# Kernel tuning notes

Hardware: AMD Instinct MI355X
Metric: run time of the kernel (lower is better)

Reference implementation:

```python
import jax, jax.numpy as jnp
import numpy as np

# ---------- constants ----------
EPS = 1e-5
_rng = np.random.default_rng(0)
_P = _rng.normal(size=(8, 3))
_P /= np.linalg.norm(_P, axis=1, keepdims=True)

def _y2_np(p):
    x, y, z = p[:, 0], p[:, 1], p[:, 2]
    return np.stack([x * y, y * z, 3 * z * z - 1, x * z, x * x - y * y], axis=-1)

_A2 = np.linalg.pinv(_y2_np(_P)).astype(np.float32)  # [5,8]
P_C = jnp.asarray(_P.astype(np.float32))
A2_C = jnp.asarray(_A2)
NORM_CONST = np.float32(1.0 / np.sqrt(20.0))  # avg_num_neighbors ** -0.5
# res update (buffer zeros, not learnable): sigmoid(0)=0.5
_U = 0.5
C_OLD = np.float32(1.0 / np.sqrt(_U * _U + 1.0))
C_NEW = np.float32(_U * C_OLD)


def _y2(p):  # real l=2 monomial basis on unit vectors
    x, y, z = p[..., 0], p[..., 1], p[..., 2]
    return jnp.stack([x * y, y * z, 3.0 * z * z - 1.0, x * z, x * x - y * y], axis=-1)


def _frame(v):  # [E,3] -> R [E,3,3] with R @ v_hat = z
    n = v / jnp.linalg.norm(v, axis=-1, keepdims=True)
    z = jnp.array([0.0, 0.0, 1.0], v.dtype)
    xa = jnp.array([1.0, 0.0, 0.0], v.dtype)
    a = jnp.where(jnp.abs(n[:, 2:3]) < 0.99, z, xa)
    e1 = jnp.cross(a, n)
    e1 = e1 / jnp.linalg.norm(e1, axis=-1, keepdims=True)
    e2 = jnp.cross(n, e1)
    return jnp.stack([e1, e2, n], axis=1)


def _wigner_d2(R):  # [E,3,3] -> D2 [E,5,5] via sample-point fit
    pts = jnp.einsum('pj,eij->epi', P_C, R)  # R @ p_k, [E,8,3]
    M = _y2(pts)  # [E,8,5] = Y_P @ D^T
    Dt = jnp.einsum('ap,epb->eab', A2_C, M)  # [E,5,5]
    return jnp.swapaxes(Dt, 1, 2)


def _sln(x, w0, b0, w1, w2):  # separable equivariant layernorm, 32x0e+16x1e+8x2e
    s = x[:, :32]
    v1 = x[:, 32:80].reshape(-1, 16, 3)
    v2 = x[:, 80:120].reshape(-1, 8, 5)
    mu = jnp.mean(s, axis=-1, keepdims=True)
    var = jnp.mean((s - mu) ** 2, axis=-1, keepdims=True)
    s = (s - mu) * jax.lax.rsqrt(var + EPS) * w0 + b0
    var1 = jnp.mean(v1 ** 2, axis=(1, 2))  # degree-balanced component variance
    var2 = jnp.mean(v2 ** 2, axis=(1, 2))
    inv = jax.lax.rsqrt(0.5 * (var1 + var2) + EPS)[:, None, None]
    v1 = v1 * inv * w1[None, :, None]
    v2 = v2 * inv * w2[None, :, None]
    return jnp.concatenate([s, v1.reshape(-1, 48), v2.reshape(-1, 40)], axis=-1)


def _ir_linear(x, W0, b0, W1, W2):  # irreps-wise linear 32x0e+16x1e+8x2e -> same
    s = x[:, :32] @ (W0 / np.sqrt(32.0)) + b0
    v1 = jnp.einsum('eui,uv->evi', x[:, 32:80].reshape(-1, 16, 3), W1) / np.sqrt(16.0)
    v2 = jnp.einsum('eui,uv->evi', x[:, 80:120].reshape(-1, 8, 5), W2) / np.sqrt(8.0)
    return jnp.concatenate([s, v1.reshape(-1, 48), v2.reshape(-1, 40)], axis=-1)


def _so2(x_cat, R, D2f, D2b, w):  # SO2 linear with per-edge dynamic weights
    E = x_cat.shape[0]
    w0 = w[:, :8960].reshape(E, 112, 80)
    w1r = w[:, 8960:10112].reshape(E, 48, 24)
    w1i = w[:, 10112:11264].reshape(E, 48, 24)
    w2r = w[:, 11264:11392].reshape(E, 16, 8)
    w2i = w[:, 11392:11520].reshape(E, 16, 8)
    # split concatenated [in + hidden] blocks
    s = jnp.concatenate([x_cat[:, :32], x_cat[:, 120:152]], axis=-1)  # [E,64]
    v1 = jnp.concatenate([x_cat[:, 32:80].reshape(E, 16, 3),
                          x_cat[:, 152:200].reshape(E, 16, 3)], axis=1)  # [E,32,3]
    v2 = jnp.concatenate([x_cat[:, 80:120].reshape(E, 8, 5),
                          x_cat[:, 200:240].reshape(E, 16 // 2, 5)], axis=1)  # [E,16,5]
    # rotate into edge-aligned frame
    v1 = jnp.einsum('eij,euj->eui', R, v1)
    v2 = jnp.einsum('eij,euj->eui', D2f, v2)
    in0 = jnp.concatenate([s, v1[:, :, 1], v2[:, :, 2]], axis=-1)   # m=0, [E,112]
    inn1 = jnp.concatenate([v1[:, :, 0], v2[:, :, 1]], axis=-1)     # m=-1, [E,48]
    inp1 = jnp.concatenate([v1[:, :, 2], v2[:, :, 3]], axis=-1)     # m=+1
    inn2 = v2[:, :, 0]  # m=-2
    inp2 = v2[:, :, 4]  # m=+2
    out0 = jnp.einsum('ei,eio->eo', in0, w0) / np.sqrt(112.0)
    op1 = (jnp.einsum('ei,eio->eo', inp1, w1r) - jnp.einsum('ei,eio->eo', inn1, w1i)) / np.sqrt(48.0)
    on1 = (jnp.einsum('ei,eio->eo', inn1, w1r) + jnp.einsum('ei,eio->eo', inp1, w1i)) / np.sqrt(48.0)
    op2 = (jnp.einsum('ei,eio->eo', inp2, w2r) - jnp.einsum('ei,eio->eo', inn2, w2i)) / np.sqrt(16.0)
    on2 = (jnp.einsum('ei,eio->eo', inn2, w2r) + jnp.einsum('ei,eio->eo', inp2, w2i)) / np.sqrt(16.0)
    s_out = out0[:, :56]
    y1 = jnp.stack([on1[:, :16], out0[:, 56:72], op1[:, :16]], axis=-1)  # [E,16,3]
    y2o = jnp.stack([on2, on1[:, 16:24], out0[:, 72:80], op1[:, 16:24], op2], axis=-1)  # [E,8,5]
    # rotate back
    y1 = jnp.einsum('eij,euj->eui', jnp.swapaxes(R, 1, 2), y1)
    y2o = jnp.einsum('eij,euj->eui', D2b, y2o)
    return jnp.concatenate([s_out, y1.reshape(E, 48), y2o.reshape(E, 40)], axis=-1)  # [E,144]


def _gate(m):  # 32x0e scalars | 24x0e gates | 16x1e+8x2e gated
    s = jax.nn.silu(m[:, :32])
    g = jax.nn.sigmoid(m[:, 32:56])
    v1 = m[:, 56:104].reshape(-1, 16, 3) * g[:, :16, None]
    v2 = m[:, 104:144].reshape(-1, 8, 5) * g[:, 16:24, None]
    return jnp.concatenate([s, v1.reshape(-1, 48), v2.reshape(-1, 40)], axis=-1)


def _env(m, we):  # E3ElementLinear: per-mul elementwise weights
    s = m[:, :32] * we[:, :32]
    v1 = m[:, 32:80].reshape(-1, 16, 3) * we[:, 32:48, None]
    v2 = m[:, 80:120].reshape(-1, 8, 5) * we[:, 48:56, None]
    return jnp.concatenate([s, v1.reshape(-1, 48), v2.reshape(-1, 40)], axis=-1)


def setup_inputs() -> dict:
    key = jax.random.key(0)
    ks = jax.random.split(key, 16)
    N, E, L = 512, 10240, 128
    inp = {
        'latents': jax.random.normal(ks[0], (E, L), jnp.float32),
        'node_features': jax.random.normal(ks[1], (N, 120), jnp.float32),
        'hidden_features': jax.random.normal(ks[2], (E, 120), jnp.float32),
        'node_onehot': jnp.ones((N, 16), jnp.float32),
        'edge_vector': jax.random.normal(ks[3], (E, 3), jnp.float32),
        'W_tp': jax.random.normal(ks[4], (L, 11520), jnp.float32),
        'W_env': jax.random.normal(ks[5], (L, 56), jnp.float32),
        'sln_w0': jnp.ones((32,), jnp.float32),
        'sln_b0': jnp.zeros((32,), jnp.float32),
        'sln_w1': jnp.ones((16,), jnp.float32),
        'sln_w2': jnp.ones((8,), jnp.float32),
        'Wp0': jax.random.normal(ks[6], (32, 32), jnp.float32),
        'bp0': jnp.zeros((32,), jnp.float32),
        'Wp1': jax.random.normal(ks[7], (16, 16), jnp.float32),
        'Wp2': jax.random.normal(ks[8], (8, 8), jnp.float32),
        'Wr0': jax.random.normal(ks[9], (32, 32), jnp.float32),
        'br0': jnp.zeros((32,), jnp.float32),
        'Wr1': jax.random.normal(ks[10], (16, 16), jnp.float32),
        'Wr2': jax.random.normal(ks[11], (8, 8), jnp.float32),
        'atom_type': jax.random.randint(ks[12], (N,), 0, 10, jnp.int32),
        'edge_index': jax.random.randint(ks[13], (2, E), 0, N, jnp.int32),
        'active_edges': jnp.arange(E, dtype=jnp.int32),
    }
    return inp


def reference(latents, node_features, hidden_features, node_onehot, edge_vector,
              W_tp, W_env, sln_w0, sln_b0, sln_w1, sln_w2,
              Wp0, bp0, Wp1, Wp2, Wr0, br0, Wr1, Wr2,
              atom_type, edge_index, active_edges):
    n_nodes = node_features.shape[0]
    center = edge_index[0][active_edges]
    nf = _sln(node_features, sln_w0, sln_b0, sln_w1, sln_w2)
    x_cat = jnp.concatenate([nf[center], hidden_features], axis=-1)  # [E,240]
    v = edge_vector[active_edges]
    R = _frame(v)
    D2f = _wigner_d2(R)
    D2b = _wigner_d2(jnp.swapaxes(R, 1, 2))
    wdyn = latents @ (W_tp / np.sqrt(128.0))  # per-edge dynamic SO2 weights
    msg = _so2(x_cat, R, D2f, D2b, wdyn)
    msg = _gate(msg)
    msg = _ir_linear(msg, Wp0, bp0, Wp1, Wp2)
    wenv = latents[active_edges] @ (W_env / np.sqrt(128.0))
    weighted = _env(msg, wenv)
    new_nf = jax.ops.segment_sum(weighted, center, num_segments=n_nodes)
    new_nf = new_nf * NORM_CONST
    res = _ir_linear(node_features, Wr0, br0, Wr1, Wr2)
    return C_NEW * new_nf + C_OLD * res
```

## Files before the change

kernel.cpp:

```cpp
#include <hip/hip_runtime.h>
#include <math.h>

#define E_TOT   10240
#define N_NODES 512
#define NCOL    11520

typedef unsigned short ushort_t;
typedef unsigned int   uint_t;
typedef __bf16 bf16x8 __attribute__((ext_vector_type(8)));
typedef float  f32x4  __attribute__((ext_vector_type(4)));

constexpr float EPSF        = 1e-5f;
constexpr float INV_SQRT128 = 0.08838834764831845f;
constexpr float INV_SQRT112 = 0.09449111825230681f;
constexpr float INV_SQRT48  = 0.14433756729740643f;
constexpr float INV_SQRT32  = 0.17677669529663687f;
constexpr float INV_SQRT16  = 0.25f;
constexpr float INV_SQRT8   = 0.35355339059327373f;
constexpr float SC0 = INV_SQRT128 * INV_SQRT112;
constexpr float SC1 = INV_SQRT128 * INV_SQRT48;
constexpr float SC2 = INV_SQRT128 * INV_SQRT16;
constexpr float C_OLD_ = 0.8944271909999159f;
constexpr float C_NEW_ = 0.4472135954999579f;
constexpr float NORMC  = 0.22360679774997896f;
constexpr float OUTSC  = C_NEW_ * NORMC;

__device__ __forceinline__ ushort_t f2bf(float x) {
  uint_t u = __float_as_uint(x);
  u = (u + 0x7fffu + ((u >> 16) & 1u)) >> 16;
  return (ushort_t)u;
}

__device__ __forceinline__ void wigner5(const float q[9], float D[25]) {
  const float q0x=q[0],q0y=q[1],q0z=q[2];
  const float q1x=q[3],q1y=q[4],q1z=q[5];
  const float q2x=q[6],q2y=q[7],q2z=q[8];
  D[0]  = q0x*q1y + q1x*q0y;
  D[1]  = q0y*q1z + q1y*q0z;
  D[2]  = 0.5f*(q0z*q1z);
  D[3]  = q0x*q1z + q1x*q0z;
  D[4]  = 0.5f*(q0x*q1x - q0y*q1y);
  D[5]  = q1x*q2y + q2x*q1y;
  D[6]  = q1y*q2z + q2y*q1z;
  D[7]  = 0.5f*(q1z*q2z);
  D[8]  = q1x*q2z + q2x*q1z;
  D[9]  = 0.5f*(q1x*q2x - q1y*q2y);
  D[10] = 6.f*q2x*q2y;
  D[11] = 6.f*q2y*q2z;
  D[12] = 0.5f*(3.f*q2z*q2z - 1.f);
  D[13] = 6.f*q2x*q2z;
  D[14] = 1.5f*(q2x*q2x - q2y*q2y);
  D[15] = q0x*q2y + q2x*q0y;
  D[16] = q0y*q2z + q2y*q0z;
  D[17] = 0.5f*(q0z*q2z);
  D[18] = q0x*q2z + q2x*q0z;
  D[19] = 0.5f*(q0x*q2x - q0y*q2y);
  D[20] = 2.f*(q0x*q0y - q1x*q1y);
  D[21] = 2.f*(q0y*q0z - q1y*q1z);
  D[22] = 0.5f*(q0z*q0z - q1z*q1z);
  D[23] = 2.f*(q0x*q0z - q1x*q1z);
  D[24] = 0.5f*((q0x*q0x - q1x*q1x) - (q0y*q0y - q1y*q1y));
}

__global__ __launch_bounds__(256)
void kAB(const float* __restrict__ Wtp, const float* __restrict__ lat,
         const float* __restrict__ Wenv,
         const float* __restrict__ ndf, const float* __restrict__ hid,
         const float* __restrict__ evec,
         const int* __restrict__ eidx, const int* __restrict__ act,
         const float* __restrict__ w0, const float* __restrict__ b0,
         const float* __restrict__ w1, const float* __restrict__ w2,
         const float* __restrict__ Wr0, const float* __restrict__ br0,
         const float* __restrict__ Wr1, const float* __restrict__ Wr2,
         ushort_t* __restrict__ Wp,
         ushort_t* __restrict__ lath, ushort_t* __restrict__ latl,
         float* __restrict__ oa_g, float* __restrict__ wenvg,
         float* __restrict__ invT, float* __restrict__ Rm,
         float* __restrict__ D2bm, float* __restrict__ out) {
  __shared__ __align__(16) char smem[47104];
  const int bid = blockIdx.x;
  const int t = threadIdx.x;
  if (bid < 720) {
    float* Wl = (float*)smem;
    const int nt = bid;
    int col, tt;
    if (nt < 560)      { col = nt/112; tt = nt - col*112; }
    else if (nt < 608) { col = 5;  tt = nt-560; }
    else if (nt < 632) { col = 6;  tt = nt-608; }
    else if (nt < 680) { col = 7;  tt = nt-632; }
    else if (nt < 704) { col = 8;  tt = nt-680; }
    else if (nt < 712) { col = 9;  tt = nt-704; }
    else               { col = 10; tt = nt-712; }
    {
      const int m1 = t & 15, lp = t >> 4;
      int c; float sc;
      switch (col) {
        case 5:  c = 8960  + tt*24 + m1;                        sc = SC1; break;
        case 6:  c = 8960  + (2*tt + (m1>>3))*24 + 16 + (m1&7); sc = SC1; break;
        case 7:  c = 10112 + tt*24 + m1;                        sc = SC1; break;
        case 8:  c = 10112 + (2*tt + (m1>>3))*24 + 16 + (m1&7); sc = SC1; break;
        case 9:  c = 11264 + (2*tt + (m1>>3))*8 + (m1&7);       sc = SC2; break;
        case 10: c = 11392 + (2*tt + (m1>>3))*8 + (m1&7);       sc = SC2; break;
        default: c = tt*80 + col*16 + m1;                       sc = SC0; break;
      }
#pragma unroll
      for (int p = 0; p < 8; ++p) {
        int l = p*16 + lp;
        Wl[l*17 + m1] = Wtp[(size_t)l*NCOL + c] * sc;
      }
    }
    __syncthreads();
    const int kc = t >> 6, lane = t & 63;
    const int m = lane & 15, kg = lane >> 4;
    ushort_t hi[8], lo[8];
#pragma unroll
    for (int jj = 0; jj < 8; ++jj) {
      int l = kc*32 + kg*8 + jj;
      float w = Wl[l*17 + m];
      ushort_t h = f2bf(w);
      float hf = __uint_as_float(((uint_t)h) << 16);
      hi[jj] = h;
      lo[jj] = f2bf(w - hf);
    }
    size_t base = ((size_t)nt*8 + kc*2)*512 + (size_t)lane*8;
    *(uint4*)&Wp[base]       = *(const uint4*)hi;
    *(uint4*)&Wp[base + 512] = *(const uint4*)lo;
    return;
  }
  if (bid < 5840) {
    const int j = bid - 720;
    const int idx = j*256 + t;
    float x = lat[idx];
    ushort_t h = f2bf(x);
    float hf = __uint_as_float(((uint_t)h) << 16);
    lath[idx] = h;
    latl[idx] = f2bf(x - hf);
#pragma unroll
    for (int i = t; i < 288; i += 256) oa_g[(size_t)j*288 + i] = 0.f;
    return;
  }
  if (bid < 6160) {
    float (*xs)[240] = (float(*)[240])smem;
    float (*Rs)[9]   = (float(*)[9])(smem + 30720);
    float (*Dfs)[25] = (float(*)[25])(smem + 31872);
    float* muS  = (float*)(smem + 35072);
    float* isS  = (float*)(smem + 35200);
    float* invS = (float*)(smem + 35328);
    int*   ctrs = (int*)(smem + 35456);
    const int e0 = (bid - 5840)*32;
    if (t < 32) {
      const int e = e0 + t;
      const int ae = act[e];
      ctrs[t] = eidx[ae];
      float vx = evec[ae*3+0], vy = evec[ae*3+1], vz = evec[ae*3+2];
      float rn = rsqrtf(vx*vx + vy*vy + vz*vz);
      float nx = vx*rn, ny = vy*rn, nz = vz*rn;
      float e1x, e1y, e1z;
      if (fabsf(nz) < 0.99f) { e1x = -ny; e1y = nx;  e1z = 0.f; }
      else                   { e1x = 0.f; e1y = -nz; e1z = ny;  }
      float rl = rsqrtf(e1x*e1x + e1y*e1y + e1z*e1z);
      e1x *= rl; e1y *= rl; e1z *= rl;
      float e2x = ny*e1z - nz*e1y;
      float e2y = nz*e1x - nx*e1z;
      float e2z = nx*e1y - ny*e1x;
      float R[9] = {e1x,e1y,e1z, e2x,e2y,e2z, nx,ny,nz};
#pragma unroll
      for (int jj = 0; jj < 9; ++jj) { Rs[t][jj] = R[jj]; Rm[(size_t)e*9 + jj] = R[jj]; }
      float Df[25];
      wigner5(R, Df);
#pragma unroll
      for (int jj = 0; jj < 25; ++jj) Dfs[t][jj] = Df[jj];
      float Rt[9] = {R[0],R[3],R[6], R[1],R[4],R[7], R[2],R[5],R[8]};
      float Db[25];
      wigner5(Rt, Db);
#pragma unroll
      for (int jj = 0; jj < 25; ++jj) D2bm[(size_t)e*25 + jj] = Db[jj];
    }
    __syncthreads();
    for (int i = t; i < 32*120; i += 256) {
      int s = i/120, jj = i - s*120;
      xs[s][jj]     = ndf[(size_t)ctrs[s]*120 + jj];
      xs[s][120+jj] = hid[(size_t)(e0+s)*120 + jj];
    }
    __syncthreads();
    if (t < 32) {
      float sum = 0.f, sq = 0.f;
#pragma unroll
      for (int i = 0; i < 32; ++i) { float v = xs[t][i]; sum += v; sq += v*v; }
      float mu = sum*(1.f/32.f);
      float var = sq*(1.f/32.f) - mu*mu;
      float v1s = 0.f, v2s = 0.f;
#pragma unroll
      for (int i = 32; i < 80; ++i) { float v = xs[t][i]; v1s += v*v; }
#pragma unroll
      for (int i = 80; i < 120; ++i) { float v = xs[t][i]; v2s += v*v; }
      muS[t] = mu;
      isS[t] = rsqrtf(var + EPSF);
      invS[t] = rsqrtf(0.5f*(v1s*(1.f/48.f) + v2s*(1.f/40.f)) + EPSF);
    }
    __syncthreads();
    const int e = t & 31, rb = t >> 5;
    const float* X  = xs[e];
    const float* Rr = Rs[e];
    const float* Df = Dfs[e];
    const float mu = muS[e], istd = isS[e], inv = invS[e];
#pragma unroll
    for (int r = rb; r < 240; r += 8) {
      float val;
      if (r < 64) {
        if (r < 32) val = (X[r] - mu)*istd*w0[r] + b0[r];
        else        val = X[88 + r];
      } else if (r < 96) {
        int u = r - 64; int b; float fac;
        if (u < 16) { b = 32 + 3*u; fac = inv*w1[u]; } else { b = 152 + 3*(u-16); fac = 1.f; }
        val = (Rr[3]*X[b] + Rr[4]*X[b+1] + Rr[5]*X[b+2])*fac;
      } else if (r < 112) {
        int u = r - 96; int b; float fac;
        if (u < 8) { b = 80 + 5*u; fac = inv*w2[u]; } else { b = 200 + 5*(u-8); fac = 1.f; }
        val = (Df[10]*X[b] + Df[11]*X[b+1] + Df[12]*X[b+2] + Df[13]*X[b+3] + Df[14]*X[b+4])*fac;
      } else if (r < 160) {
        int u = r - 112;
        if (u < 32) {
          int b; float fac;
          if (u < 16) { b = 32 + 3*u; fac = inv*w1[u]; } else { b = 152 + 3*(u-16); fac = 1.f; }
          val = (Rr[0]*X[b] + Rr[1]*X[b+1] + Rr[2]*X[b+2])*fac;
        } else {
          int u2 = u - 32; int b; float fac;
          if (u2 < 8) { b = 80 + 5*u2; fac = inv*w2[u2]; } else { b = 200 + 5*(u2-8); fac = 1.f; }
          val = (Df[5]*X[b] + Df[6]*X[b+1] + Df[7]*X[b+2] + Df[8]*X[b+3] + Df[9]*X[b+4])*fac;
        }
      } else if (r < 208) {
        int u = r - 160;
        if (u < 32) {
          int b; float fac;
          if (u < 16) { b = 32 + 3*u; fac = inv*w1[u]; } else { b = 152 + 3*(u-16); fac = 1.f; }
          val = (Rr[6]*X[b] + Rr[7]*X[b+1] + Rr[8]*X[b+2])*fac;
        } else {
          int u2 = u - 32; int b; float fac;
          if (u2 < 8) { b = 80 + 5*u2; fac = inv*w2[u2]; } else { b = 200 + 5*(u2-8); fac = 1.f; }
          val = (Df[15]*X[b] + Df[16]*X[b+1] + Df[17]*X[b+2] + Df[18]*X[b+3] + Df[19]*X[b+4])*fac;
        }
      } else if (r < 224) {
        int u = r - 208; int b; float fac;
        if (u < 8) { b = 80 + 5*u; fac = inv*w2[u]; } else { b = 200 + 5*(u-8); fac = 1.f; }
        val = (Df[0]*X[b] + Df[1]*X[b+1] + Df[2]*X[b+2] + Df[3]*X[b+3] + Df[4]*X[b+4])*fac;
      } else {
        int u = r - 224; int b; float fac;
        if (u < 8) { b = 80 + 5*u; fac = inv*w2[u]; } else { b = 200 + 5*(u-8); fac = 1.f; }
        val = (Df[20]*X[b] + Df[21]*X[b+1] + Df[22]*X[b+2] + Df[23]*X[b+3] + Df[24]*X[b+4])*fac;
      }
      invT[(size_t)r*E_TOT + e0 + e] = val;
    }
    return;
  }
  if (bid < 6672) {
    const int n = bid - 6160;
    if (t >= 120) return;
    const float* x = ndf + (size_t)n*120;
    float r;
    if (t < 32) {
      float s = 0.f;
#pragma unroll
      for (int i = 0; i < 32; ++i) s += x[i]*Wr0[i*32 + t];
      r = s*INV_SQRT32 + br0[t];
    } else if (t < 80) {
      int j = t - 32, v = j/3, cp = j - 3*v;
      float s = 0.f;
#pragma unroll
      for (int u = 0; u < 16; ++u) s += x[32 + u*3 + cp]*Wr1[u*16 + v];
      r = s*INV_SQRT16;
    } else {
      int j = t - 80, v = j/5, cp = j - 5*v;
      float s = 0.f;
#pragma unroll
      for (int u = 0; u < 8; ++u) s += x[80 + u*5 + cp]*Wr2[u*8 + v];
      r = s*INV_SQRT8;
    }
    out[(size_t)n*120 + t] = C_OLD_*r;
    return;
  }
  {
    float* Wl2  = (float*)smem;
    float* latc = (float*)(smem + 28672);
    int*   aes  = (int*)(smem + 46080);
    const int e0 = (bid - 6672)*256;
    for (int i = t; i < 128*56; i += 256) Wl2[i] = Wenv[i];
    aes[t] = act[e0 + t];
    float acc[56];
#pragma unroll
    for (int o = 0; o < 56; ++o) acc[o] = 0.f;
    for (int lc = 0; lc < 8; ++lc) {
      __syncthreads();
      for (int i = t; i < 256*16; i += 256) {
        int el = i >> 4, j = i & 15;
        latc[el*17 + j] = lat[(size_t)aes[el]*128 + lc*16 + j];
      }
      __syncthreads();
#pragma unroll
      for (int j = 0; j < 16; ++j) {
        float lv = latc[t*17 + j];
        const float* wr = &Wl2[(lc*16 + j)*56];
#pragma unroll
        for (int o = 0; o < 56; ++o) acc[o] += lv * wr[o];
      }
    }
    float* dst = wenvg + (size_t)(e0 + t)*56;
#pragma unroll
    for (int o = 0; o < 56; ++o) dst[o] = acc[o] * INV_SQRT128;
  }
}

struct Seg { int col, tt, mP, mN, sP, sN, segLen; float sg; bool PAIR, TWO; };
__device__ __forceinline__ void setp(Seg& s) {
  const int cf = s.col;
  if (cf < 5)       { s.segLen=112; s.mP=0;   s.mN=0;   s.sP=cf*16; s.sN=0;   s.sg=1.f;  s.PAIR=false; s.TWO=false; }
  else if (cf == 5) { s.segLen=48;  s.mP=160; s.mN=112; s.sP=80;  s.sN=104; s.sg=1.f;  s.PAIR=false; s.TWO=true; }
  else if (cf == 6) { s.segLen=24;  s.mP=160; s.mN=112; s.sP=96;  s.sN=120; s.sg=1.f;  s.PAIR=true;  s.TWO=true; }
  else if (cf == 7) { s.segLen=48;  s.mP=112; s.mN=160; s.sP=80;  s.sN=104; s.sg=-1.f; s.PAIR=false; s.TWO=true; }
  else if (cf == 8) { s.segLen=24;  s.mP=112; s.mN=160; s.sP=96;  s.sN=120; s.sg=-1.f; s.PAIR=true;  s.TWO=true; }
  else if (cf == 9) { s.segLen=8;   s.mP=224; s.mN=208; s.sP=128; s.sN=136; s.sg=1.f;  s.PAIR=true;  s.TWO=true; }
  else              { s.segLen=8;   s.mP=208; s.mN=224; s.sP=128; s.sN=136; s.sg=-1.f; s.PAIR=true;  s.TWO=true; }
}
__device__ __forceinline__ bool adv(Seg& s) {
  s.tt++;
  if (s.tt == s.segLen) { s.col++; s.tt = 0; setp(s); return true; }
  return false;
}

__global__ __launch_bounds__(256, 3)
void k3_gemm(const ushort_t* __restrict__ Wp,
             const ushort_t* __restrict__ lath,
             const ushort_t* __restrict__ latl,
             const float*  __restrict__ invT,
             float* __restrict__ oa_g) {
  __shared__ __align__(16) ushort_t abuf[2][8192];
  const int t = threadIdx.x;
  const int wave = t >> 6, lane = t & 63;
  const int le = lane & 15, g = lane >> 4, gh = g >> 1;
  const int fbase = blockIdx.y * 80;
  const int e0w = blockIdx.x*128 + wave*32;
  bf16x8 Bh[4][2], Bl[4][2];
#pragma unroll
  for (int kc = 0; kc < 4; ++kc)
#pragma unroll
    for (int n = 0; n < 2; ++n) {
      size_t off = (size_t)(e0w + n*16 + le)*128 + kc*32 + g*8;
      Bh[kc][n] = *(const bf16x8*)(lath + off);
      Bl[kc][n] = *(const bf16x8*)(latl + off);
    }
  Seg s;
  if (fbase < 560)      { s.col = fbase/112; s.tt = fbase - s.col*112; }
  else if (fbase < 608) { s.col = 5;  s.tt = fbase-560; }
  else if (fbase < 632) { s.col = 6;  s.tt = fbase-608; }
  else if (fbase < 680) { s.col = 7;  s.tt = fbase-632; }
  else if (fbase < 704) { s.col = 8;  s.tt = fbase-680; }
  else if (fbase < 712) { s.col = 9;  s.tt = fbase-704; }
  else                  { s.col = 10; s.tt = fbase-712; }
  setp(s);
  auto loadG = [&](const Seg& q, float& p0, float& p1, float& n0, float& n1) {
    int idx = q.PAIR ? (2*q.tt + gh) : q.tt;
    p0 = invT[(size_t)(q.mP + idx)*E_TOT + e0w + le];
    p1 = invT[(size_t)(q.mP + idx)*E_TOT + e0w + 16 + le];
    if (q.TWO) {
      n0 = invT[(size_t)(q.mN + idx)*E_TOT + e0w + le];
      n1 = invT[(size_t)(q.mN + idx)*E_TOT + e0w + 16 + le];
    } else { n0 = 0.f; n1 = 0.f; }
  };
  f32x4 aP0={0,0,0,0}, aP1={0,0,0,0}, aN0={0,0,0,0}, aN1={0,0,0,0};
  auto flushSeg = [&](const Seg& fs) {
#pragma unroll
    for (int r = 0; r < 4; ++r) {
      int mm = g*4 + r;
      int sp = fs.sP + (fs.PAIR ? (mm & 7) : mm);
      atomicAdd(&oa_g[(size_t)(e0w + le)*144 + sp], fs.sg*aP0[r]);
      atomicAdd(&oa_g[(size_t)(e0w + 16 + le)*144 + sp], fs.sg*aP1[r]);
      if (fs.TWO) {
        int sn = fs.sN + (fs.PAIR ? (mm & 7) : mm);
        atomicAdd(&oa_g[(size_t)(e0w + le)*144 + sn], aN0[r]);
        atomicAdd(&oa_g[(size_t)(e0w + 16 + le)*144 + sn], aN1[r]);
      }
    }
    aP0 = (f32x4){0,0,0,0}; aP1 = (f32x4){0,0,0,0};
    aN0 = (f32x4){0,0,0,0}; aN1 = (f32x4){0,0,0,0};
  };
#pragma unroll
  for (int qq = 0; qq < 4; ++qq) {
    uint4 v = *(const uint4*)(Wp + ((size_t)fbase*8 + wave*4 + qq)*512 + lane*8);
    *(uint4*)&abuf[0][(wave*4 + qq)*512 + lane*8] = v;
  }
  float cP0[2], cP1[2], cN0[2], cN1[2];
  {
    Seg t0 = s; Seg t1 = s; adv(t1);
    loadG(t0, cP0[0], cP1[0], cN0[0], cN1[0]);
    loadG(t1, cP0[1], cP1[1], cN0[1], cN1[1]);
  }
  __syncthreads();
  for (int c = 0; c < 40; ++c) {
    const int cb = c & 1, nb = cb ^ 1;
    uint4 pre[4];
    const bool more = (c + 1) < 40;
    float nP0[2], nP1[2], nN0[2], nN1[2];
    if (more) {
#pragma unroll
      for (int qq = 0; qq < 4; ++qq)
        pre[qq] = *(const uint4*)(Wp + ((size_t)(fbase + 2*(c+1))*8 + wave*4 + qq)*512 + lane*8);
      Seg t0 = s; adv(t0); adv(t0);
      Seg t1 = t0; adv(t1);
      loadG(t0, nP0[0], nP1[0], nN0[0], nN1[0]);
      loadG(t1, nP0[1], nP1[1], nN0[1], nN1[1]);
    }
    Seg s1 = s;
    const bool cross0 = adv(s1);
    {
      f32x4 dE0={0,0,0,0}, dO0={0,0,0,0}, dE1={0,0,0,0}, dO1={0,0,0,0};
#pragma unroll
      for (int kc = 0; kc < 2; ++kc) {
        bf16x8 Ah = *(const bf16x8*)&abuf[cb][(kc*2 + 0)*512 + lane*8];
        bf16x8 Al = *(const bf16x8*)&abuf[cb][(kc*2 + 1)*512 + lane*8];
        dE0 = __builtin_amdgcn_mfma_f32_16x16x32_bf16(Ah, Bh[kc][0], dE0, 0, 0, 0);
        dE1 = __builtin_amdgcn_mfma_f32_16x16x32_bf16(Ah, Bh[kc][1], dE1, 0, 0, 0);
        dE0 = __builtin_amdgcn_mfma_f32_16x16x32_bf16(Ah, Bl[kc][0], dE0, 0, 0, 0);
        dE1 = __builtin_amdgcn_mfma_f32_16x16x32_bf16(Ah, Bl[kc][1], dE1, 0, 0, 0);
        dE0 = __builtin_amdgcn_mfma_f32_16x16x32_bf16(Al, Bh[kc][0], dE0, 0, 0, 0);
        dE1 = __builtin_amdgcn_mfma_f32_16x16x32_bf16(Al, Bh[kc][1], dE1, 0, 0, 0);
      }
#pragma unroll
      for (int kc = 2; kc < 4; ++kc) {
        bf16x8 Ah = *(const bf16x8*)&abuf[cb][(kc*2 + 0)*512 + lane*8];
        bf16x8 Al = *(const bf16x8*)&abuf[cb][(kc*2 + 1)*512 + lane*8];
        dO0 = __builtin_amdgcn_mfma_f32_16x16x32_bf16(Ah, Bh[kc][0], dO0, 0, 0, 0);
        dO1 = __builtin_amdgcn_mfma_f32_16x16x32_bf16(Ah, Bh[kc][1], dO1, 0, 0, 0);
        dO0 = __builtin_amdgcn_mfma_f32_16x16x32_bf16(Ah, Bl[kc][0], dO0, 0, 0, 0);
        dO1 = __builtin_amdgcn_mfma_f32_16x16x32_bf16(Ah, Bl[kc][1], dO1, 0, 0, 0);
        dO0 = __builtin_amdgcn_mfma_f32_16x16x32_bf16(Al, Bh[kc][0], dO0, 0, 0, 0);
        dO1 = __builtin_amdgcn_mfma_f32_16x16x32_bf16(Al, Bh[kc][1], dO1, 0, 0, 0);
      }
      f32x4 d0 = dE0 + dO0, d1 = dE1 + dO1;
#pragma unroll
      for (int r = 0; r < 4; ++r) { aP0[r] += cP0[0]*d0[r]; aP1[r] += cP1[0]*d1[r]; }
      if (s.TWO) {
#pragma unroll
        for (int r = 0; r < 4; ++r) { aN0[r] += cN0[0]*d0[r]; aN1[r] += cN1[0]*d1[r]; }
      }
    }
    if (cross0) flushSeg(s);
    {
      f32x4 dE0={0,0,0,0}, dO0={0,0,0,0}, dE1={0,0,0,0}, dO1={0,0,0,0};
#pragma unroll
      for (int kc = 0; kc < 2; ++kc) {
        bf16x8 Ah = *(const bf16x8*)&abuf[cb][(8 + kc*2 + 0)*512 + lane*8];
        bf16x8 Al = *(const bf16x8*)&abuf[cb][(8 + kc*2 + 1)*512 + lane*8];
        dE0 = __builtin_amdgcn_mfma_f32_16x16x32_bf16(Ah, Bh[kc][0], dE0, 0, 0, 0);
        dE1 = __builtin_amdgcn_mfma_f32_16x16x32_bf16(Ah, Bh[kc][1], dE1, 0, 0, 0);
        dE0 = __builtin_amdgcn_mfma_f32_16x16x32_bf16(Ah, Bl[kc][0], dE0, 0, 0, 0);
        dE1 = __builtin_amdgcn_mfma_f32_16x16x32_bf16(Ah, Bl[kc][1], dE1, 0, 0, 0);
        dE0 = __builtin_amdgcn_mfma_f32_16x16x32_bf16(Al, Bh[kc][0], dE0, 0, 0, 0);
        dE1 = __builtin_amdgcn_mfma_f32_16x16x32_bf16(Al, Bh[kc][1], dE1, 0, 0, 0);
      }
#pragma unroll
      for (int kc = 2; kc < 4; ++kc) {
        bf16x8 Ah = *(const bf16x8*)&abuf[cb][(8 + kc*2 + 0)*512 + lane*8];
        bf16x8 Al = *(const bf16x8*)&abuf[cb][(8 + kc*2 + 1)*512 + lane*8];
        dO0 = __builtin_amdgcn_mfma_f32_16x16x32_bf16(Ah, Bh[kc][0], dO0, 0, 0, 0);
        dO1 = __builtin_amdgcn_mfma_f32_16x16x32_bf16(Ah, Bh[kc][1], dO1, 0, 0, 0);
        dO0 = __builtin_amdgcn_mfma_f32_16x16x32_bf16(Ah, Bl[kc][0], dO0, 0, 0, 0);
        dO1 = __builtin_amdgcn_mfma_f32_16x16x32_bf16(Ah, Bl[kc][1], dO1, 0, 0, 0);
        dO0 = __builtin_amdgcn_mfma_f32_16x16x32_bf16(Al, Bh[kc][0], dO0, 0, 0, 0);
        dO1 = __builtin_amdgcn_mfma_f32_16x16x32_bf16(Al, Bh[kc][1], dO1, 0, 0, 0);
      }
      f32x4 d0 = dE0 + dO0, d1 = dE1 + dO1;
#pragma unroll
      for (int r = 0; r < 4; ++r) { aP0[r] += cP0[1]*d0[r]; aP1[r] += cP1[1]*d1[r]; }
      if (s1.TWO) {
#pragma unroll
        for (int r = 0; r < 4; ++r) { aN0[r] += cN0[1]*d0[r]; aN1[r] += cN1[1]*d1[r]; }
      }
    }
    {
      Seg s2 = s1;
      const bool cross1 = adv(s2);
      if (cross1) flushSeg(s1);
      s = s2;
    }
#pragma unroll
    for (int q2 = 0; q2 < 2; ++q2) {
      cP0[q2] = nP0[q2]; cP1[q2] = nP1[q2];
      cN0[q2] = nN0[q2]; cN1[q2] = nN1[q2];
    }
    if (more) {
#pragma unroll
      for (int qq = 0; qq < 4; ++qq)
        *(uint4*)&abuf[nb][(wave*4 + qq)*512 + lane*8] = pre[qq];
    }
    __syncthreads();
  }
  if (s.tt > 0) flushSeg(s);
}

__global__ __launch_bounds__(256)
void k4_epi(const float* __restrict__ oa_g, const float* __restrict__ Rm,
            const float* __restrict__ D2bm, const float* __restrict__ wenvg,
            const int* __restrict__ eidx, const int* __restrict__ act,
            const float* __restrict__ Wp0, const float* __restrict__ bp0,
            const float* __restrict__ Wp1, const float* __restrict__ Wp2,
            float* __restrict__ out) {
  __shared__ float sc[4][200];
  const int wave = threadIdx.x >> 6, lane = threadIdx.x & 63;
  const int eg = blockIdx.x*4 + wave;
  const int ae = act[eg];
  const float* o_ = oa_g + (size_t)eg*144;
  if (lane < 56) {
    sc[wave][144 + lane] = wenvg[(size_t)eg*56 + lane];
    float v = o_[lane];
    sc[wave][lane] = (lane < 32) ? v/(1.f + expf(-v)) : 1.f/(1.f + expf(-v));
  }
  __syncthreads();
  const float* Rr = Rm + (size_t)eg*9;
  const float* Db = D2bm + (size_t)eg*25;
  if (lane < 48) {
    int u = lane/3, cc = lane - u*3;
    float yx = o_[104+u], yy = o_[56+u], yz = o_[80+u];
    float p = Rr[cc]*yx + Rr[3+cc]*yy + Rr[6+cc]*yz;
    sc[wave][56+lane] = p * sc[wave][32+u];
  }
  __syncthreads();
  if (lane < 40) {
    int u = lane/5, ii = lane - u*5;
    float y0 = o_[136+u], y1v = o_[120+u], y2v = o_[72+u], y3 = o_[96+u], y4 = o_[128+u];
    float p = Db[ii*5+0]*y0 + Db[ii*5+1]*y1v + Db[ii*5+2]*y2v + Db[ii*5+3]*y3 + Db[ii*5+4]*y4;
    sc[wave][104+lane] = p * sc[wave][48+u];
  }
  __syncthreads();
  const int ctr = eidx[ae];
  float* dst = out + (size_t)ctr*120;
  const float* we = &sc[wave][144];
#pragma unroll
  for (int rnd = 0; rnd < 2; ++rnd) {
    int jo = rnd*64 + lane;
    if (jo < 120) {
      float val;
      if (jo < 32) {
        float s = 0.f;
#pragma unroll
        for (int i2 = 0; i2 < 32; ++i2) s += sc[wave][i2]*Wp0[i2*32 + jo];
        val = (s*INV_SQRT32 + bp0[jo]) * we[jo];
      } else if (jo < 80) {
        int jj = jo-32, v = jj/3, cc = jj - v*3;
        float s = 0.f;
#pragma unroll
        for (int u = 0; u < 16; ++u) s += sc[wave][56 + u*3 + cc]*Wp1[u*16 + v];
        val = s*INV_SQRT16*we[32+v];
      } else {
        int jj = jo-80, v = jj/5, ii = jj - v*5;
        float s = 0.f;
#pragma unroll
        for (int u = 0; u < 8; ++u) s += sc[wave][104 + u*5 + ii]*Wp2[u*8 + v];
        val = s*INV_SQRT8*we[48+v];
      }
      atomicAdd(&dst[jo], OUTSC*val);
    }
  }
}

extern "C" void kernel_launch(void* const* d_in, const int* in_sizes, int n_in,
                              void* d_out, int out_size, void* d_ws, size_t ws_size,
                              hipStream_t stream) {
  const float* lat  = (const float*)d_in[0];
  const float* ndf  = (const float*)d_in[1];
  const float* hid  = (const float*)d_in[2];
  const float* evec = (const float*)d_in[4];
  const float* Wtp  = (const float*)d_in[5];
  const float* Wenv = (const float*)d_in[6];
  const float* w0   = (const float*)d_in[7];
  const float* b0   = (const float*)d_in[8];
  const float* w1   = (const float*)d_in[9];
  const float* w2   = (const float*)d_in[10];
  const float* Wp0  = (const float*)d_in[11];
  const float* bp0  = (const float*)d_in[12];
  const float* Wp1  = (const float*)d_in[13];
  const float* Wp2  = (const float*)d_in[14];
  const float* Wr0  = (const float*)d_in[15];
  const float* br0  = (const float*)d_in[16];
  const float* Wr1  = (const float*)d_in[17];
  const float* Wr2  = (const float*)d_in[18];
  const int*   eidx = (const int*)d_in[20];
  const int*   act  = (const int*)d_in[21];
  float* out = (float*)d_out;

  char* p = (char*)d_ws;
  float*    invT  = (float*)(p + 245760);
  float*    Rm    = (float*)(p + 10076160);
  float*    D2bm  = (float*)(p + 10444800);
  float*    wenvg = (float*)(p + 11468800);
  float*    oa_g  = (float*)(p + 14008320);
  ushort_t* lath  = (ushort_t*)(p + 19906560);
  ushort_t* latl  = (ushort_t*)(p + 22528000);
  ushort_t* Wpack = (ushort_t*)(p + 25149440);

  kAB<<<6712, 256, 0, stream>>>(Wtp, lat, Wenv, ndf, hid, evec, eidx, act,
                                w0, b0, w1, w2, Wr0, br0, Wr1, Wr2,
                                Wpack, lath, latl, oa_g, wenvg, invT, Rm, D2bm, out);
  k3_gemm<<<dim3(E_TOT/128, 9), 256, 0, stream>>>(Wpack, lath, latl, invT, oa_g);
  k4_epi<<<E_TOT/4, 256, 0, stream>>>(oa_g, Rm, D2bm, wenvg, eidx, act,
                                      Wp0, bp0, Wp1, Wp2, out);
}
```

Measured before the change: 284.2 us.

## Fuse epilogue into GEMM via last-block-done counter and regrid to eight slices

```diff
diff --git a/kernel.cpp b/kernel.cpp
--- a/kernel.cpp
+++ b/kernel.cpp
@@ -76,7 +76,8 @@
          ushort_t* __restrict__ lath, ushort_t* __restrict__ latl,
          float* __restrict__ oa_g, float* __restrict__ wenvg,
          float* __restrict__ invT, float* __restrict__ Rm,
-         float* __restrict__ D2bm, float* __restrict__ out) {
+         float* __restrict__ D2bm, float* __restrict__ out,
+         int* __restrict__ cnt) {
   __shared__ __align__(16) char smem[47104];
   const int bid = blockIdx.x;
   const int t = threadIdx.x;
@@ -137,6 +138,7 @@
     latl[idx] = f2bf(x - hf);
 #pragma unroll
     for (int i = t; i < 288; i += 256) oa_g[(size_t)j*288 + i] = 0.f;
+    if (j == 0 && t < 80) cnt[t] = 0;
     return;
   }
   if (bid < 6160) {
@@ -327,18 +329,26 @@
   return false;
 }
 
-__global__ __launch_bounds__(256, 3)
+__global__ __launch_bounds__(256, 2)
 void k3_gemm(const ushort_t* __restrict__ Wp,
              const ushort_t* __restrict__ lath,
              const ushort_t* __restrict__ latl,
              const float*  __restrict__ invT,
-             float* __restrict__ oa_g) {
+             float* __restrict__ oa_g,
+             const float* __restrict__ Rm, const float* __restrict__ D2bm,
+             const float* __restrict__ wenvg,
+             const int* __restrict__ eidx, const int* __restrict__ act,
+             const float* __restrict__ Wp0, const float* __restrict__ bp0,
+             const float* __restrict__ Wp1, const float* __restrict__ Wp2,
+             float* __restrict__ out, int* __restrict__ cnt) {
   __shared__ __align__(16) ushort_t abuf[2][8192];
+  __shared__ int lastFlag;
   const int t = threadIdx.x;
   const int wave = t >> 6, lane = t & 63;
   const int le = lane & 15, g = lane >> 4, gh = g >> 1;
-  const int fbase = blockIdx.y * 80;
-  const int e0w = blockIdx.x*128 + wave*32;
+  const int bx = blockIdx.x >> 3, by = blockIdx.x & 7;
+  const int fbase = by * 90;
+  const int e0w = bx*128 + wave*32;
   bf16x8 Bh[4][2], Bl[4][2];
 #pragma unroll
   for (int kc = 0; kc < 4; ++kc)
@@ -395,10 +405,10 @@
     loadG(t1, cP0[1], cP1[1], cN0[1], cN1[1]);
   }
   __syncthreads();
-  for (int c = 0; c < 40; ++c) {
+  for (int c = 0; c < 45; ++c) {
     const int cb = c & 1, nb = cb ^ 1;
     uint4 pre[4];
-    const bool more = (c + 1) < 40;
+    const bool more = (c + 1) < 45;
     float nP0[2], nP1[2], nN0[2], nN1[2];
     if (more) {
 #pragma unroll
@@ -495,70 +505,76 @@
     __syncthreads();
   }
   if (s.tt > 0) flushSeg(s);
-}
-
-__global__ __launch_bounds__(256)
-void k4_epi(const float* __restrict__ oa_g, const float* __restrict__ Rm,
-            const float* __restrict__ D2bm, const float* __restrict__ wenvg,
-            const int* __restrict__ eidx, const int* __restrict__ act,
-            const float* __restrict__ Wp0, const float* __restrict__ bp0,
-            const float* __restrict__ Wp1, const float* __restrict__ Wp2,
-            float* __restrict__ out) {
-  __shared__ float sc[4][200];
-  const int wave = threadIdx.x >> 6, lane = threadIdx.x & 63;
-  const int eg = blockIdx.x*4 + wave;
-  const int ae = act[eg];
-  const float* o_ = oa_g + (size_t)eg*144;
-  if (lane < 56) {
-    sc[wave][144 + lane] = wenvg[(size_t)eg*56 + lane];
-    float v = o_[lane];
-    sc[wave][lane] = (lane < 32) ? v/(1.f + expf(-v)) : 1.f/(1.f + expf(-v));
-  }
+
+  __threadfence();
   __syncthreads();
-  const float* Rr = Rm + (size_t)eg*9;
-  const float* Db = D2bm + (size_t)eg*25;
-  if (lane < 48) {
-    int u = lane/3, cc = lane - u*3;
-    float yx = o_[104+u], yy = o_[56+u], yz = o_[80+u];
-    float p = Rr[cc]*yx + Rr[3+cc]*yy + Rr[6+cc]*yz;
-    sc[wave][56+lane] = p * sc[wave][32+u];
-  }
+  if (t == 0) lastFlag = (atomicAdd(&cnt[bx], 1) == 7);
   __syncthreads();
-  if (lane < 40) {
-    int u = lane/5, ii = lane - u*5;
-    float y0 = o_[136+u], y1v = o_[120+u], y2v = o_[72+u], y3 = o_[96+u], y4 = o_[128+u];
-    float p = Db[ii*5+0]*y0 + Db[ii*5+1]*y1v + Db[ii*5+2]*y2v + Db[ii*5+3]*y3 + Db[ii*5+4]*y4;
-    sc[wave][104+lane] = p * sc[wave][48+u];
-  }
-  __syncthreads();
-  const int ctr = eidx[ae];
-  float* dst = out + (size_t)ctr*120;
-  const float* we = &sc[wave][144];
-#pragma unroll
-  for (int rnd = 0; rnd < 2; ++rnd) {
-    int jo = rnd*64 + lane;
-    if (jo < 120) {
-      float val;
-      if (jo < 32) {
-        float s = 0.f;
-#pragma unroll
-        for (int i2 = 0; i2 < 32; ++i2) s += sc[wave][i2]*Wp0[i2*32 + jo];
-        val = (s*INV_SQRT32 + bp0[jo]) * we[jo];
-      } else if (jo < 80) {
-        int jj = jo-32, v = jj/3, cc = jj - v*3;
-        float s = 0.f;
-#pragma unroll
-        for (int u = 0; u < 16; ++u) s += sc[wave][56 + u*3 + cc]*Wp1[u*16 + v];
-        val = s*INV_SQRT16*we[32+v];
-      } else {
-        int jj = jo-80, v = jj/5, ii = jj - v*5;
-        float s = 0.f;
-#pragma unroll
-        for (int u = 0; u < 8; ++u) s += sc[wave][104 + u*5 + ii]*Wp2[u*8 + v];
-        val = s*INV_SQRT8*we[48+v];
-      }
-      atomicAdd(&dst[jo], OUTSC*val);
-    }
+  if (!lastFlag) return;
+  __threadfence();
+
+  float* eps = (float*)abuf;
+  float* oaw = eps + wave*384;
+  float* scw = oaw + 144;
+  for (int it = 0; it < 32; ++it) {
+    const int eg = bx*128 + wave*32 + it;
+    const int ae = act[eg];
+    for (int i = lane; i < 144; i += 64)
+      oaw[i] = __hip_atomic_load(&oa_g[(size_t)eg*144 + i],
+                                 __ATOMIC_RELAXED, __HIP_MEMORY_SCOPE_AGENT);
+    __syncthreads();
+    if (lane < 56) {
+      scw[144 + lane] = wenvg[(size_t)eg*56 + lane];
+      float v = oaw[lane];
+      scw[lane] = (lane < 32) ? v/(1.f + expf(-v)) : 1.f/(1.f + expf(-v));
+    }
+    __syncthreads();
+    const float* Rr = Rm + (size_t)eg*9;
+    const float* Db = D2bm + (size_t)eg*25;
+    if (lane < 48) {
+      int u = lane/3, cc = lane - u*3;
+      float yx = oaw[104+u], yy = oaw[56+u], yz = oaw[80+u];
+      float pv = Rr[cc]*yx + Rr[3+cc]*yy + Rr[6+cc]*yz;
+      scw[56+lane] = pv * scw[32+u];
+    }
+    __syncthreads();
+    if (lane < 40) {
+      int u = lane/5, ii = lane - u*5;
+      float y0 = oaw[136+u], y1v = oaw[120+u], y2v = oaw[72+u], y3 = oaw[96+u], y4 = oaw[128+u];
+      float pv = Db[ii*5+0]*y0 + Db[ii*5+1]*y1v + Db[ii*5+2]*y2v + Db[ii*5+3]*y3 + Db[ii*5+4]*y4;
+      scw[104+lane] = pv * scw[48+u];
+    }
+    __syncthreads();
+    const int ctr = eidx[ae];
+    float* dst = out + (size_t)ctr*120;
+    const float* we = &scw[144];
+#pragma unroll
+    for (int rnd = 0; rnd < 2; ++rnd) {
+      int jo = rnd*64 + lane;
+      if (jo < 120) {
+        float val;
+        if (jo < 32) {
+          float ss = 0.f;
+#pragma unroll
+          for (int i2 = 0; i2 < 32; ++i2) ss += scw[i2]*Wp0[i2*32 + jo];
+          val = (ss*INV_SQRT32 + bp0[jo]) * we[jo];
+        } else if (jo < 80) {
+          int jj = jo-32, v = jj/3, cc = jj - v*3;
+          float ss = 0.f;
+#pragma unroll
+          for (int u = 0; u < 16; ++u) ss += scw[56 + u*3 + cc]*Wp1[u*16 + v];
+          val = ss*INV_SQRT16*we[32+v];
+        } else {
+          int jj = jo-80, v = jj/5, ii = jj - v*5;
+          float ss = 0.f;
+#pragma unroll
+          for (int u = 0; u < 8; ++u) ss += scw[104 + u*5 + ii]*Wp2[u*8 + v];
+          val = ss*INV_SQRT8*we[48+v];
+        }
+        atomicAdd(&dst[jo], OUTSC*val);
+      }
+    }
+    __syncthreads();
   }
 }
 
@@ -592,6 +608,7 @@
   float*    Rm    = (float*)(p + 10076160);
   float*    D2bm  = (float*)(p + 10444800);
   float*    wenvg = (float*)(p + 11468800);
+  int*      cnt   = (int*)(p + 13762560);
   float*    oa_g  = (float*)(p + 14008320);
   ushort_t* lath  = (ushort_t*)(p + 19906560);
   ushort_t* latl  = (ushort_t*)(p + 22528000);
@@ -599,8 +616,9 @@
 
   kAB<<<6712, 256, 0, stream>>>(Wtp, lat, Wenv, ndf, hid, evec, eidx, act,
                                 w0, b0, w1, w2, Wr0, br0, Wr1, Wr2,
-                                Wpack, lath, latl, oa_g, wenvg, invT, Rm, D2bm, out);
-  k3_gemm<<<dim3(E_TOT/128, 9), 256, 0, stream>>>(Wpack, lath, latl, invT, oa_g);
-  k4_epi<<<E_TOT/4, 256, 0, stream>>>(oa_g, Rm, D2bm, wenvg, eidx, act,
-                                      Wp0, bp0, Wp1, Wp2, out);
+                                Wpack, lath, latl, oa_g, wenvg, invT, Rm, D2bm,
+                                out, cnt);
+  k3_gemm<<<640, 256, 0, stream>>>(Wpack, lath, latl, invT, oa_g,
+                                   Rm, D2bm, wenvg, eidx, act,
+                                   Wp0, bp0, Wp1, Wp2, out, cnt);
 }
```

New measurement: 513.5 us. +80.7%, slower.
